# Performance work log

Measured on AMD Instinct MI355X. Metric: run time of the kernel, lower is better.

The kernel has to match this reference:

```python
import jax, jax.numpy as jnp
import numpy as np
import math

D = 2048
NH = 16
HD = D // NH
MULT = 4
EPS = 1e-6


def rmsnorm(x, g):
    norm = jax.lax.rsqrt(jnp.mean(x * x, axis=-1, keepdims=True) + EPS)
    return g * x * norm


def setup_inputs() -> dict:
    key = jax.random.key(0)
    ks = jax.random.split(key, 8)
    s = 0.02  # keep activations in a sane range
    return {
        "x": jax.random.normal(ks[0], (2, 2048, D), dtype=jnp.float32),
        "g1": jnp.ones((D,), dtype=jnp.float32),
        "wq": jax.random.normal(ks[1], (D, D), dtype=jnp.float32) * s,
        "wk": jax.random.normal(ks[2], (D, D), dtype=jnp.float32) * s,
        "wv": jax.random.normal(ks[3], (D, D), dtype=jnp.float32) * s,
        "wo": jax.random.normal(ks[4], (D, D), dtype=jnp.float32) * s,
        "g2": jnp.ones((D,), dtype=jnp.float32),
        "w_up": jax.random.normal(ks[5], (2 * D * MULT, D), dtype=jnp.float32) * s,
        "w_down": jax.random.normal(ks[6], (D, D * MULT), dtype=jnp.float32) * s,
    }


def reference(x, g1, wq, wk, wv, wo, g2, w_up, w_down):
    B, T, _ = x.shape
    # --- causal self-attention with pre-RMSNorm ---
    h = rmsnorm(x, g1)
    q = (h @ wq.T).reshape(B, T, NH, HD).transpose(0, 2, 1, 3)  # [B,H,T,hd]
    k = (h @ wk.T).reshape(B, T, NH, HD).transpose(0, 2, 1, 3)
    v = (h @ wv.T).reshape(B, T, NH, HD).transpose(0, 2, 1, 3)
    att = jnp.einsum("bhtd,bhsd->bhts", q, k) / math.sqrt(HD)  # [B,H,T,T]
    neg = jnp.finfo(att.dtype).min
    causal = jnp.triu(jnp.full((T, T), neg, dtype=att.dtype), k=1)
    att = att + causal
    w = jax.nn.softmax(att, axis=-1)
    z = jnp.einsum("bhts,bhsd->bhtd", w, v)  # [B,H,T,hd]
    z = z.transpose(0, 2, 1, 3).reshape(B, T, D)
    x = x + z @ wo.T
    # --- SwiGLU-style FFN (GELU gate) with pre-RMSNorm ---
    h2 = rmsnorm(x, g2)
    uv = h2 @ w_up.T  # [B,T,2*D*MULT]
    u, vgate = jnp.split(uv, 2, axis=-1)
    ff = (jax.nn.gelu(u, approximate=False) * vgate) @ w_down.T
    return x + ff
```

## Files before the change

### kernel.cpp

```cpp
#include <hip/hip_runtime.h>
#include <math.h>

typedef __bf16 bf16_t;
typedef __bf16 bf16x8 __attribute__((ext_vector_type(8)));
typedef __bf16 bf16x4 __attribute__((ext_vector_type(4)));
typedef float f32x4 __attribute__((ext_vector_type(4)));

#define D_MODEL 2048
#define N_HEADS 16
#define HEAD_D 128
#define SEQ 2048
#define NTOK 4096
#define DFF 8192
#define UPN 16384

#define GLDS16(g, l) __builtin_amdgcn_global_load_lds( \
    (const __attribute__((address_space(1))) void*)(g), \
    (__attribute__((address_space(3))) void*)(l), 16, 0, 0)

#define MFMA16(a, b, c) __builtin_amdgcn_mfma_f32_16x16x32_bf16((a), (b), (c), 0, 0, 0)

__global__ __launch_bounds__(256) void cvt_bf16_kernel(const float* __restrict__ in,
                                                       bf16_t* __restrict__ out, long n4) {
    long i = (long)blockIdx.x * 256 + threadIdx.x;
    long stride = (long)gridDim.x * 256;
    for (; i < n4; i += stride) {
        float4 f = ((const float4*)in)[i];
        bf16x4 v;
        v[0] = (bf16_t)f.x; v[1] = (bf16_t)f.y; v[2] = (bf16_t)f.z; v[3] = (bf16_t)f.w;
        ((bf16x4*)out)[i] = v;
    }
}

__global__ __launch_bounds__(256) void rmsnorm_kernel(const float* __restrict__ x,
                                                      const float* __restrict__ g,
                                                      bf16_t* __restrict__ out) {
    int row = blockIdx.x;
    const float* xr = x + (size_t)row * D_MODEL;
    int c0 = threadIdx.x * 8;
    float4 a = *(const float4*)&xr[c0];
    float4 b = *(const float4*)&xr[c0 + 4];
    float ss = a.x*a.x + a.y*a.y + a.z*a.z + a.w*a.w
             + b.x*b.x + b.y*b.y + b.z*b.z + b.w*b.w;
    #pragma unroll
    for (int off = 1; off < 64; off <<= 1) ss += __shfl_xor(ss, off);
    __shared__ float red[4];
    if ((threadIdx.x & 63) == 0) red[threadIdx.x >> 6] = ss;
    __syncthreads();
    float norm = rsqrtf((red[0] + red[1] + red[2] + red[3]) * (1.f / D_MODEL) + 1e-6f);
    float4 ga = *(const float4*)&g[c0];
    float4 gb = *(const float4*)&g[c0 + 4];
    bf16x8 o;
    o[0] = (bf16_t)(a.x * ga.x * norm); o[1] = (bf16_t)(a.y * ga.y * norm);
    o[2] = (bf16_t)(a.z * ga.z * norm); o[3] = (bf16_t)(a.w * ga.w * norm);
    o[4] = (bf16_t)(b.x * gb.x * norm); o[5] = (bf16_t)(b.y * gb.y * norm);
    o[6] = (bf16_t)(b.z * gb.z * norm); o[7] = (bf16_t)(b.w * gb.w * norm);
    *(bf16x8*)&out[(size_t)row * D_MODEL + c0] = o;
}

__global__ __launch_bounds__(256) void combine3_kernel(const float* __restrict__ r,
        const float* __restrict__ p0, const float* __restrict__ p1,
        float* __restrict__ out, long n4) {
    long i = (long)blockIdx.x * 256 + threadIdx.x;
    long stride = (long)gridDim.x * 256;
    for (; i < n4; i += stride) {
        float4 a = ((const float4*)r)[i];
        float4 b = ((const float4*)p0)[i];
        float4 c = ((const float4*)p1)[i];
        float4 o; o.x = a.x+b.x+c.x; o.y = a.y+b.y+c.y; o.z = a.z+b.z+c.z; o.w = a.w+b.w+c.w;
        ((float4*)out)[i] = o;
    }
}

template<int MODE, int KSPLIT>
__global__ __launch_bounds__(512, 2)
void gemm256(const bf16_t* __restrict__ A, const bf16_t* __restrict__ W,
             void* __restrict__ o0, void* __restrict__ o1, void* __restrict__ o2,
             const float* __restrict__ res, int nbx, int K)
{
    __shared__ __align__(16) bf16_t ldsA[2 * 2 * 8192];
    __shared__ __align__(16) bf16_t ldsB[2 * 2 * 8192];
    const int tid = threadIdx.x;
    const int wave = tid >> 6, lane = tid & 63;
    const int lr = lane & 15, lg = lane >> 4;
    const int wm = wave >> 2, wn = wave & 3;

    const int nwg = gridDim.x, bid = blockIdx.x;
    const int cpx = nwg >> 3;
    const int s = (bid & 7) * cpx + (bid >> 3);
    const int by = s & 15, bx = s >> 4;
    const int bm0 = by * 256;
    const int bn0 = (MODE == 2) ? bx * 128 : bx * 256;
    const int z = (KSPLIT == 2) ? blockIdx.z : 0;
    const int Keff = K / KSPLIT, koff = z * Keff;

    const int rl = wave * 16 + (lane >> 2);
    const int gsw = ((lane & 3) ^ ((rl >> 1) & 3)) * 8;
    const bf16_t* asrc = A + (size_t)(bm0 + rl) * K + koff + gsw;
    const bf16_t* bsrc;
    size_t bstep2;
    if constexpr (MODE == 2) {
        int grp = rl >> 6, wi = rl & 63;
        int brow = (wi < 32) ? (bn0 + grp * 32 + wi) : (DFF + bn0 + grp * 32 + (wi - 32));
        bsrc = W + (size_t)brow * K + koff + gsw;
        bstep2 = (size_t)64 * K;
    } else {
        bsrc = W + (size_t)(bn0 + rl) * K + koff + gsw;
        bstep2 = (size_t)128 * K;
    }

    auto stA = [&](int t, int kh) {
        char* d = (char*)ldsA + (((t & 1) * 2 + kh) * 16384) + wave * 1024 + lane * 16;
        const bf16_t* sp = asrc + (size_t)t * 64 + kh * 32;
        GLDS16(sp, d);
        GLDS16(sp + (size_t)128 * K, d + 8192);
    };
    auto stB = [&](int t, int kh) {
        char* d = (char*)ldsB + (((t & 1) * 2 + kh) * 16384) + wave * 1024 + lane * 16;
        const bf16_t* sp = bsrc + (size_t)t * 64 + kh * 32;
        GLDS16(sp, d);
        GLDS16(sp + bstep2, d + 8192);
    };

    f32x4 acc[8][4] = {};
    const int xg = (lg ^ ((lr >> 1) & 3)) * 8;
    const int NKT = Keff >> 6;

    stA(0, 0); stB(0, 0); stA(0, 1); stB(0, 1); stA(1, 0); stB(1, 0);
    asm volatile("s_waitcnt vmcnt(8)" ::: "memory");
    __builtin_amdgcn_s_barrier();

#define TILE_BODY(T, S1, S2, W1, W2)                                                    \
    {                                                                                   \
        const int t_ = (T);                                                             \
        const bf16_t* Ab = ldsA + ((t_ & 1) * 2) * 8192;                                \
        const bf16_t* Bb = ldsB + ((t_ & 1) * 2) * 8192;                                \
        bf16x8 a0[4], a1[4], b0[4], b1[4];                                              \
                                                                      \
        _Pragma("unroll")                                                               \
        for (int i = 0; i < 4; ++i)                                                     \
            a0[i] = *(const bf16x8*)&Ab[(wm * 128 + i * 16 + lr) * 32 + xg];            \
        _Pragma("unroll")                                                               \
        for (int n = 0; n < 4; ++n)                                                     \
            b0[n] = *(const bf16x8*)&Bb[(wn * 64 + n * 16 + lr) * 32 + xg];             \
        if (S1) stA(t_ + 1, 1);                                                         \
        __builtin_amdgcn_s_setprio(1);                                                  \
        _Pragma("unroll")                                                               \
        for (int i = 0; i < 4; ++i)                                                     \
            _Pragma("unroll")                                                           \
            for (int n = 0; n < 4; ++n)                                                 \
                acc[i][n] = MFMA16(a0[i], b0[n], acc[i][n]);                            \
        __builtin_amdgcn_s_setprio(0);                                                  \
                                                                      \
        _Pragma("unroll")                                                               \
        for (int i = 0; i < 4; ++i)                                                     \
            a1[i] = *(const bf16x8*)&Ab[(wm * 128 + (i + 4) * 16 + lr) * 32 + xg];      \
        if (S1) stB(t_ + 1, 1);                                                         \
        __builtin_amdgcn_s_setprio(1);                                                  \
        _Pragma("unroll")                                                               \
        for (int i = 0; i < 4; ++i)                                                     \
            _Pragma("unroll")                                                           \
            for (int n = 0; n < 4; ++n)                                                 \
                acc[i + 4][n] = MFMA16(a1[i], b0[n], acc[i + 4][n]);                    \
        __builtin_amdgcn_s_setprio(0);                                                  \
        asm volatile("s_waitcnt vmcnt(" W1 ")" ::: "memory");                           \
        __builtin_amdgcn_s_barrier();                                                   \
                                                                      \
        _Pragma("unroll")                                                               \
        for (int i = 0; i < 4; ++i)                                                     \
            a0[i] = *(const bf16x8*)&Ab[8192 + (wm * 128 + i * 16 + lr) * 32 + xg];     \
        _Pragma("unroll")                                                               \
        for (int n = 0; n < 4; ++n)                                                     \
            b1[n] = *(const bf16x8*)&Bb[8192 + (wn * 64 + n * 16 + lr) * 32 + xg];      \
        if (S2) stA(t_ + 2, 0);                                                         \
        __builtin_amdgcn_s_setprio(1);                                                  \
        _Pragma("unroll")                                                               \
        for (int i = 0; i < 4; ++i)                                                     \
            _Pragma("unroll")                                                           \
            for (int n = 0; n < 4; ++n)                                                 \
                acc[i][n] = MFMA16(a0[i], b1[n], acc[i][n]);                            \
        __builtin_amdgcn_s_setprio(0);                                                  \
                                                                      \
        _Pragma("unroll")                                                               \
        for (int i = 0; i < 4; ++i)                                                     \
            a1[i] = *(const bf16x8*)&Ab[8192 + (wm * 128 + (i + 4) * 16 + lr) * 32 + xg]; \
        if (S2) stB(t_ + 2, 0);                                                         \
        __builtin_amdgcn_s_setprio(1);                                                  \
        _Pragma("unroll")                                                               \
        for (int i = 0; i < 4; ++i)                                                     \
            _Pragma("unroll")                                                           \
            for (int n = 0; n < 4; ++n)                                                 \
                acc[i + 4][n] = MFMA16(a1[i], b1[n], acc[i + 4][n]);                    \
        __builtin_amdgcn_s_setprio(0);                                                  \
        asm volatile("s_waitcnt vmcnt(" W2 ")" ::: "memory");                           \
        __builtin_amdgcn_s_barrier();                                                   \
    }

    for (int t = 0; t < NKT - 2; ++t) TILE_BODY(t, true, true, "8", "8");
    TILE_BODY(NKT - 2, true, false, "8", "4");
    TILE_BODY(NKT - 1, false, false, "0", "0");
#undef TILE_BODY

    if constexpr (MODE == 0) {
        const float qs = 0.08838834764831845f;
        const int th = bn0 >> 11;
        #pragma unroll
        for (int m = 0; m < 8; ++m) {
            int grow = bm0 + wm * 128 + m * 16 + lg * 4;
            #pragma unroll
            for (int n = 0; n < 4; ++n) {
                int gcol = bn0 + wn * 64 + n * 16 + lr;
                int c = gcol & 2047;
                if (th == 0) {
                    #pragma unroll
                    for (int r = 0; r < 4; ++r)
                        ((bf16_t*)o0)[(size_t)(grow + r) * D_MODEL + c] = (bf16_t)(acc[m][n][r] * qs);
                } else if (th == 1) {
                    #pragma unroll
                    for (int r = 0; r < 4; ++r)
                        ((bf16_t*)o1)[(size_t)(grow + r) * D_MODEL + c] = (bf16_t)acc[m][n][r];
                } else {
                    int hh = c >> 7, d = c & 127;
                    int bb = grow >> 11, t0 = grow & 2047;
                    bf16x4 st;
                    #pragma unroll
                    for (int r = 0; r < 4; ++r) st[r] = (bf16_t)acc[m][n][r];
                    *(bf16x4*)&((bf16_t*)o2)[((size_t)(bb * N_HEADS + hh) * HEAD_D + d) * SEQ + t0] = st;
                }
            }
        }
    } else if constexpr (MODE == 1) {
        float* po = (KSPLIT == 2) ? ((float*)o0 + (size_t)z * NTOK * D_MODEL) : (float*)o0;
        #pragma unroll
        for (int m = 0; m < 8; ++m) {
            int grow = bm0 + wm * 128 + m * 16 + lg * 4;
            #pragma unroll
            for (int n = 0; n < 4; ++n) {
                int gcol = bn0 + wn * 64 + n * 16 + lr;
                #pragma unroll
                for (int r = 0; r < 4; ++r) {
                    size_t idx = (size_t)(grow + r) * D_MODEL + gcol;
                    if (KSPLIT == 2) po[idx] = acc[m][n][r];
                    else             po[idx] = res[idx] + acc[m][n][r];
                }
            }
        }
    } else {
        #pragma unroll
        for (int m = 0; m < 8; ++m) {
            int grow = bm0 + wm * 128 + m * 16 + lg * 4;
            #pragma unroll
            for (int n = 0; n < 2; ++n) {
                int gcol = bn0 + wn * 32 + n * 16 + lr;
                #pragma unroll
                for (int r = 0; r < 4; ++r) {
                    float u = acc[m][n][r], vg = acc[m][n + 2][r];
                    float ge = 0.5f * u * (1.f + erff(u * 0.70710678118654752f));
                    ((bf16_t*)o0)[(size_t)(grow + r) * DFF + gcol] = (bf16_t)(ge * vg);
                }
            }
        }
    }
}

__global__ __launch_bounds__(256)
void attn_kernel(const bf16_t* __restrict__ Q, const bf16_t* __restrict__ K,
                 const bf16_t* __restrict__ Vt, bf16_t* __restrict__ Z)
{
    const int qt = gridDim.x - 1 - blockIdx.x;
    const int h = blockIdx.y, b = blockIdx.z;
    const int q0 = qt * 64;
    const int tid = threadIdx.x, wave = tid >> 6, lane = tid & 63;
    const int lr = lane & 15, lg = lane >> 4;

    __shared__ __align__(16) bf16_t Qs[64 * 136];
    __shared__ __align__(16) bf16_t Ks[64 * 136];
    __shared__ __align__(16) bf16_t Vts[128 * 72];
    __shared__ __align__(16) bf16_t Ps[4][16 * 72];

    const size_t base = ((size_t)b * SEQ) * D_MODEL + (size_t)h * HEAD_D;
    const size_t vbase = (size_t)(b * N_HEADS + h) * HEAD_D * SEQ;

    #pragma unroll
    for (int i = 0; i < 4; ++i) {
        int v = tid + 256 * i;
        int row = v >> 4, cv = (v & 15) * 8;
        *(uint4*)&Qs[row * 136 + cv] = *(const uint4*)&Q[base + (size_t)(q0 + row) * D_MODEL + cv];
    }

    f32x4 o[8] = {};
    float mrun[4], lrun[4];
    #pragma unroll
    for (int r = 0; r < 4; ++r) { mrun[r] = -1e30f; lrun[r] = 0.f; }

    for (int kt = 0; kt <= qt; ++kt) {
        const int k0 = kt * 64;
        __syncthreads();
        #pragma unroll
        for (int i = 0; i < 4; ++i) {
            int v = tid + 256 * i;
            int row = v >> 4, cv = (v & 15) * 8;
            *(uint4*)&Ks[row * 136 + cv] = *(const uint4*)&K[base + (size_t)(k0 + row) * D_MODEL + cv];
            int d = v >> 3, c8 = (v & 7) * 8;
            *(uint4*)&Vts[d * 72 + c8] = *(const uint4*)&Vt[vbase + (size_t)d * SEQ + k0 + c8];
        }
        __syncthreads();

        f32x4 sv[4] = {};
        #pragma unroll
        for (int kk = 0; kk < 4; ++kk) {
            bf16x8 aq = *(const bf16x8*)&Qs[(wave * 16 + lr) * 136 + kk * 32 + lg * 8];
            #pragma unroll
            for (int nb = 0; nb < 4; ++nb) {
                bf16x8 bk = *(const bf16x8*)&Ks[(nb * 16 + lr) * 136 + kk * 32 + lg * 8];
                sv[nb] = MFMA16(aq, bk, sv[nb]);
            }
        }
        if (kt == qt) {
            #pragma unroll
            for (int nb = 0; nb < 4; ++nb)
                #pragma unroll
                for (int r = 0; r < 4; ++r) {
                    int qrel = 16 * wave + lg * 4 + r;
                    int krel = nb * 16 + lr;
                    if (krel > qrel) sv[nb][r] = -1e30f;
                }
        }
        float resc[4];
        #pragma unroll
        for (int r = 0; r < 4; ++r) {
            float mx = fmaxf(fmaxf(sv[0][r], sv[1][r]), fmaxf(sv[2][r], sv[3][r]));
            #pragma unroll
            for (int off = 1; off < 16; off <<= 1) mx = fmaxf(mx, __shfl_xor(mx, off));
            float mnew = fmaxf(mrun[r], mx);
            resc[r] = __expf(mrun[r] - mnew);
            float sum = 0.f;
            #pragma unroll
            for (int nb = 0; nb < 4; ++nb) {
                float p = __expf(sv[nb][r] - mnew);
                sv[nb][r] = p;
                sum += p;
            }
            #pragma unroll
            for (int off = 1; off < 16; off <<= 1) sum += __shfl_xor(sum, off);
            lrun[r] = lrun[r] * resc[r] + sum;
            mrun[r] = mnew;
        }
        #pragma unroll
        for (int ob = 0; ob < 8; ++ob)
            #pragma unroll
            for (int r = 0; r < 4; ++r) o[ob][r] *= resc[r];
        #pragma unroll
        for (int nb = 0; nb < 4; ++nb)
            #pragma unroll
            for (int r = 0; r < 4; ++r)
                Ps[wave][(lg * 4 + r) * 72 + nb * 16 + lr] = (bf16_t)sv[nb][r];
        #pragma unroll
        for (int kk = 0; kk < 2; ++kk) {
            bf16x8 ap = *(const bf16x8*)&Ps[wave][lr * 72 + kk * 32 + lg * 8];
            #pragma unroll
            for (int ob = 0; ob < 8; ++ob) {
                bf16x8 bv = *(const bf16x8*)&Vts[(ob * 16 + lr) * 72 + kk * 32 + lg * 8];
                o[ob] = MFMA16(ap, bv, o[ob]);
            }
        }
    }
    #pragma unroll
    for (int ob = 0; ob < 8; ++ob)
        #pragma unroll
        for (int r = 0; r < 4; ++r) {
            int t = q0 + 16 * wave + lg * 4 + r;
            Z[base + (size_t)t * D_MODEL + ob * 16 + lr] = (bf16_t)(o[ob][r] / lrun[r]);
        }
}

extern "C" void kernel_launch(void* const* d_in, const int* in_sizes, int n_in,
                              void* d_out, int out_size, void* d_ws, size_t ws_size,
                              hipStream_t stream)
{
    const float* x   = (const float*)d_in[0];
    const float* g1  = (const float*)d_in[1];
    const float* wq  = (const float*)d_in[2];
    const float* wk  = (const float*)d_in[3];
    const float* wv  = (const float*)d_in[4];
    const float* wo  = (const float*)d_in[5];
    const float* g2  = (const float*)d_in[6];
    const float* wup = (const float*)d_in[7];
    const float* wdn = (const float*)d_in[8];
    float* out = (float*)d_out;

    char* wsp = (char*)d_ws;
    size_t off = 0;
    auto alloc = [&](size_t bytes) { void* p = wsp + off; off += (bytes + 255) & ~255ull; return p; };
    bf16_t* wq_b  = (bf16_t*)alloc((size_t)D_MODEL * D_MODEL * 2);
    bf16_t* wk_b  = (bf16_t*)alloc((size_t)D_MODEL * D_MODEL * 2);
    bf16_t* wv_b  = (bf16_t*)alloc((size_t)D_MODEL * D_MODEL * 2);
    bf16_t* wo_b  = (bf16_t*)alloc((size_t)D_MODEL * D_MODEL * 2);
    bf16_t* wup_b = (bf16_t*)alloc((size_t)UPN * D_MODEL * 2);
    bf16_t* wdn_b = (bf16_t*)alloc((size_t)D_MODEL * DFF * 2);
    bf16_t* h_b   = (bf16_t*)alloc((size_t)NTOK * D_MODEL * 2);
    bf16_t* q_b   = (bf16_t*)alloc((size_t)NTOK * D_MODEL * 2);
    bf16_t* k_b   = (bf16_t*)alloc((size_t)NTOK * D_MODEL * 2);
    bf16_t* vt_b  = (bf16_t*)alloc((size_t)NTOK * D_MODEL * 2);
    bf16_t* z_b   = (bf16_t*)alloc((size_t)NTOK * D_MODEL * 2);
    float*  x1    = (float*) alloc((size_t)NTOK * D_MODEL * 4);
    bf16_t* h2_b  = (bf16_t*)alloc((size_t)NTOK * D_MODEL * 2);
    bf16_t* act_b = (bf16_t*)alloc((size_t)NTOK * DFF * 2);
    float* pbuf = (float*)h_b;

    auto cvt = [&](const float* in, bf16_t* outb, long n) {
        long n4 = n / 4;
        long nb = (n4 + 255) / 256;
        int blocks = nb > 2048 ? 2048 : (int)nb;
        cvt_bf16_kernel<<<blocks, 256, 0, stream>>>(in, outb, n4);
    };
    cvt(wq,  wq_b,  (long)D_MODEL * D_MODEL);
    cvt(wk,  wk_b,  (long)D_MODEL * D_MODEL);
    cvt(wv,  wv_b,  (long)D_MODEL * D_MODEL);
    cvt(wo,  wo_b,  (long)D_MODEL * D_MODEL);
    cvt(wup, wup_b, (long)UPN * D_MODEL);
    cvt(wdn, wdn_b, (long)D_MODEL * DFF);

    rmsnorm_kernel<<<NTOK, 256, 0, stream>>>(x, g1, h_b);

    gemm256<0, 1><<<24 * 16, 512, 0, stream>>>(h_b, wq_b, q_b, k_b, vt_b, nullptr, 24, D_MODEL);

    attn_kernel<<<dim3(SEQ / 64, N_HEADS, 2), 256, 0, stream>>>(q_b, k_b, vt_b, z_b);

    gemm256<1, 2><<<dim3(8 * 16, 1, 2), 512, 0, stream>>>(z_b, wo_b, pbuf, nullptr, nullptr, nullptr, 8, D_MODEL);
    combine3_kernel<<<2048, 256, 0, stream>>>(x, pbuf, pbuf + (size_t)NTOK * D_MODEL, x1,
                                              (long)NTOK * D_MODEL / 4);

    rmsnorm_kernel<<<NTOK, 256, 0, stream>>>(x1, g2, h2_b);

    gemm256<2, 1><<<64 * 16, 512, 0, stream>>>(h2_b, wup_b, act_b, nullptr, nullptr, nullptr, 64, D_MODEL);

    gemm256<1, 2><<<dim3(8 * 16, 1, 2), 512, 0, stream>>>(act_b, wdn_b, pbuf, nullptr, nullptr, nullptr, 8, DFF);
    combine3_kernel<<<2048, 256, 0, stream>>>(x1, pbuf, pbuf + (size_t)NTOK * D_MODEL, out,
                                              (long)NTOK * D_MODEL / 4);
}
```

Measured before the change: 968.3 us.

## Prefetch next K/V tile into registers and defer softmax rescaling in attention

The attention kernel now loads the next K and V^T tile into registers while the current tile is being computed, which hides global-memory latency behind the MFMA work. Online softmax skips the running-max update and the rescaling of the output accumulator when the new max does not exceed the old one by more than 8 across the wave (the FA4-style lazy rescale). The final normalisation multiplies by a reciprocal instead of dividing. The register prefetch raises register pressure, and deferred max updates allow exp values up to e^8, which can cost some bf16 precision in P.

```diff
diff --git a/kernel.cpp b/kernel.cpp
--- a/kernel.cpp
+++ b/kernel.cpp
@@ -281,12 +281,28 @@
     const size_t base = ((size_t)b * SEQ) * D_MODEL + (size_t)h * HEAD_D;
     const size_t vbase = (size_t)(b * N_HEADS + h) * HEAD_D * SEQ;
 
+    int krow[4], kcv[4], vd[4], vc8[4];
     #pragma unroll
     for (int i = 0; i < 4; ++i) {
         int v = tid + 256 * i;
-        int row = v >> 4, cv = (v & 15) * 8;
-        *(uint4*)&Qs[row * 136 + cv] = *(const uint4*)&Q[base + (size_t)(q0 + row) * D_MODEL + cv];
-    }
+        krow[i] = v >> 4; kcv[i] = (v & 15) * 8;
+        vd[i]   = v >> 3; vc8[i] = (v & 7) * 8;
+    }
+
+    #pragma unroll
+    for (int i = 0; i < 4; ++i)
+        *(uint4*)&Qs[krow[i] * 136 + kcv[i]] = *(const uint4*)&Q[base + (size_t)(q0 + krow[i]) * D_MODEL + kcv[i]];
+
+    uint4 kreg[4], vreg[4];
+    auto loadKV = [&](int kt) {
+        const int k0 = kt * 64;
+        #pragma unroll
+        for (int i = 0; i < 4; ++i) {
+            kreg[i] = *(const uint4*)&K[base + (size_t)(k0 + krow[i]) * D_MODEL + kcv[i]];
+            vreg[i] = *(const uint4*)&Vt[vbase + (size_t)vd[i] * SEQ + k0 + vc8[i]];
+        }
+    };
+    loadKV(0);
 
     f32x4 o[8] = {};
     float mrun[4], lrun[4];
@@ -294,17 +310,14 @@
     for (int r = 0; r < 4; ++r) { mrun[r] = -1e30f; lrun[r] = 0.f; }
 
     for (int kt = 0; kt <= qt; ++kt) {
-        const int k0 = kt * 64;
         __syncthreads();
         #pragma unroll
         for (int i = 0; i < 4; ++i) {
-            int v = tid + 256 * i;
-            int row = v >> 4, cv = (v & 15) * 8;
-            *(uint4*)&Ks[row * 136 + cv] = *(const uint4*)&K[base + (size_t)(k0 + row) * D_MODEL + cv];
-            int d = v >> 3, c8 = (v & 7) * 8;
-            *(uint4*)&Vts[d * 72 + c8] = *(const uint4*)&Vt[vbase + (size_t)d * SEQ + k0 + c8];
+            *(uint4*)&Ks[krow[i] * 136 + kcv[i]] = kreg[i];
+            *(uint4*)&Vts[vd[i] * 72 + vc8[i]] = vreg[i];
         }
         __syncthreads();
+        if (kt < qt) loadKV(kt + 1);
 
         f32x4 sv[4] = {};
         #pragma unroll
@@ -327,13 +340,16 @@
                 }
         }
         float resc[4];
+        bool defer_all = true;
         #pragma unroll
         for (int r = 0; r < 4; ++r) {
             float mx = fmaxf(fmaxf(sv[0][r], sv[1][r]), fmaxf(sv[2][r], sv[3][r]));
             #pragma unroll
             for (int off = 1; off < 16; off <<= 1) mx = fmaxf(mx, __shfl_xor(mx, off));
-            float mnew = fmaxf(mrun[r], mx);
-            resc[r] = __expf(mrun[r] - mnew);
+            bool defer = __all(mx - mrun[r] <= 8.f);
+            float mnew = defer ? mrun[r] : fmaxf(mrun[r], mx);
+            resc[r] = defer ? 1.f : __expf(mrun[r] - mnew);
+            defer_all &= defer;
             float sum = 0.f;
             #pragma unroll
             for (int nb = 0; nb < 4; ++nb) {
@@ -346,10 +362,12 @@
             lrun[r] = lrun[r] * resc[r] + sum;
             mrun[r] = mnew;
         }
-        #pragma unroll
-        for (int ob = 0; ob < 8; ++ob)
-            #pragma unroll
-            for (int r = 0; r < 4; ++r) o[ob][r] *= resc[r];
+        if (!defer_all) {
+            #pragma unroll
+            for (int ob = 0; ob < 8; ++ob)
+                #pragma unroll
+                for (int r = 0; r < 4; ++r) o[ob][r] *= resc[r];
+        }
         #pragma unroll
         for (int nb = 0; nb < 4; ++nb)
             #pragma unroll
@@ -366,11 +384,13 @@
         }
     }
     #pragma unroll
+    for (int r = 0; r < 4; ++r) lrun[r] = 1.f / lrun[r];
+    #pragma unroll
     for (int ob = 0; ob < 8; ++ob)
         #pragma unroll
         for (int r = 0; r < 4; ++r) {
             int t = q0 + 16 * wave + lg * 4 + r;
-            Z[base + (size_t)t * D_MODEL + ob * 16 + lr] = (bf16_t)(o[ob][r] / lrun[r]);
+            Z[base + (size_t)t * D_MODEL + ob * 16 + lr] = (bf16_t)(o[ob][r] * lrun[r]);
         }
 }
 
```

New measurement: 1.046 ms. 1.08x slower.
